# Optimization experiments

Hardware: AMD Instinct MI355X
Metric: run time of the kernel (lower is better)

Reference implementation:

```python
import jax, jax.numpy as jnp
import numpy as np

HID = 2048   # hidden_size
NH = 16      # num_heads
HD = 128     # head_dim
R = 16       # compression_ratio
WIN = 128    # window_size
ROPE = HD // 2  # partial rope dim (resolve_rope_dim with use_partial_rope)
EPS = 1e-6


def rmsnorm(x, w):
    return x * jax.lax.rsqrt(jnp.mean(x * x, axis=-1, keepdims=True) + EPS) * w


def apply_rope(x, pos):
    # x: [..., S, D]; rotate first ROPE dims, pass the rest through.
    half = ROPE // 2
    inv_freq = 1.0 / (10000.0 ** (jnp.arange(half, dtype=jnp.float32) * 2.0 / ROPE))
    ang = pos.astype(jnp.float32)[:, None] * inv_freq[None, :]   # [S, half]
    cos, sin = jnp.cos(ang), jnp.sin(ang)
    x1, x2, rest = x[..., :half], x[..., half:ROPE], x[..., ROPE:]
    return jnp.concatenate([x1 * cos - x2 * sin, x1 * sin + x2 * cos, rest], axis=-1)


def setup_inputs() -> dict:
    key = jax.random.key(0)
    ks = jax.random.split(key, 16)
    s = 0.02
    return {
        "hidden_states": jax.random.normal(ks[0], (1, 2048, HID), jnp.float32),
        "Wq": jax.random.normal(ks[1], (HID, NH * HD), jnp.float32) * s,
        "bq": jnp.zeros((NH * HD,), jnp.float32),
        "Wc": jax.random.normal(ks[2], (HID, 1), jnp.float32) * s,   # learned compressor scores
        "bc": jnp.zeros((1,), jnp.float32),
        "Wk": jax.random.normal(ks[3], (HID, HD), jnp.float32) * s,  # shared compressed KV head
        "bk": jnp.zeros((HD,), jnp.float32),
        "Wv": jax.random.normal(ks[4], (HID, HD), jnp.float32) * s,
        "bv": jnp.zeros((HD,), jnp.float32),
        "Wlk": jax.random.normal(ks[5], (HID, NH * HD), jnp.float32) * s,
        "blk": jnp.zeros((NH * HD,), jnp.float32),
        "Wlv": jax.random.normal(ks[6], (HID, NH * HD), jnp.float32) * s,
        "blv": jnp.zeros((NH * HD,), jnp.float32),
        "qn_w": jnp.ones((HD,), jnp.float32),
        "kn_w": jnp.ones((HD,), jnp.float32),
        "sink_k": jax.random.normal(ks[7], (NH, HD), jnp.float32) * s,
        "sink_v": jax.random.normal(ks[8], (NH, HD), jnp.float32) * s,
        "Wo": jax.random.normal(ks[9], (NH * HD, HID), jnp.float32) * s,
        "bo": jnp.zeros((HID,), jnp.float32),
    }


def reference(hidden_states, Wq, bq, Wc, bc, Wk, bk, Wv, bv, Wlk, blk, Wlv, blv,
              qn_w, kn_w, sink_k, sink_v, Wo, bo):
    B, S, _ = hidden_states.shape
    pos = jnp.arange(S)
    scale = 1.0 / jnp.sqrt(jnp.float32(HD))

    # queries: proj -> heads -> RMSNorm -> partial RoPE
    q = (hidden_states @ Wq + bq).reshape(B, S, NH, HD).transpose(0, 2, 1, 3)  # [B,NH,S,HD]
    q = apply_rope(rmsnorm(q, qn_w), pos)

    # learned weighted KV compression: softmax over each block of R tokens
    C = S // R
    w = jax.nn.softmax((hidden_states @ Wc + bc).reshape(B, C, R), axis=-1)   # [B,C,R]
    entries = jnp.einsum('bcr,bcrh->bch', w, hidden_states.reshape(B, C, R, HID))
    block_ends = jnp.arange(C) * R + (R - 1)

    ck = apply_rope(rmsnorm(entries @ Wk + bk, kn_w), block_ends)  # [B,C,HD] (shared head)
    cv = entries @ Wv + bv                                         # [B,C,HD]

    # dense attention over compressed entries + learnable sink slot
    cs = jnp.einsum('bhsd,bcd->bhsc', q, ck) * scale               # [B,NH,S,C]
    cmask = block_ends[None, :] <= pos[:, None]                    # block fully in past
    cs = jnp.where(cmask, cs, -1e9)
    sink_s = jnp.einsum('bhsd,hd->bhs', q, sink_k) * scale         # sink always attendable
    attn = jax.nn.softmax(jnp.concatenate([cs, sink_s[..., None]], axis=-1), axis=-1)
    ctx_c = (jnp.einsum('bhsc,bcd->bhsd', attn[..., :C], cv)
             + attn[..., C:] * sink_v[None, :, None, :])

    # local sliding-window attention branch
    lk = (hidden_states @ Wlk + blk).reshape(B, S, NH, HD).transpose(0, 2, 1, 3)
    lk = apply_rope(rmsnorm(lk, kn_w), pos)
    lv = (hidden_states @ Wlv + blv).reshape(B, S, NH, HD).transpose(0, 2, 1, 3)
    ls = jnp.einsum('bhsd,bhtd->bhst', q, lk) * scale
    d = pos[:, None] - pos[None, :]
    lmask = (d >= 0) & (d <= WIN)
    lattn = jax.nn.softmax(jnp.where(lmask, ls, -1e9), axis=-1)
    ctx_l = jnp.einsum('bhst,bhtd->bhsd', lattn, lv)

    merged = 0.5 * (ctx_c + ctx_l)                                 # mean over 2 branches
    out = merged.transpose(0, 2, 1, 3).reshape(B, S, NH * HD) @ Wo + bo
    return out
```

## Files before the change

### kernel.cpp

```cpp
#include <hip/hip_runtime.h>


typedef unsigned short u16;
typedef __attribute__((ext_vector_type(8))) short short8;
typedef __attribute__((ext_vector_type(4))) float f32x4;

#define S_LEN 2048
#define HIDN  2048
#define NHEAD 16
#define HDIM  128
#define NCHNK 128
#define NKT   32
#define SCALE 0.08838834764831845f

__device__ __forceinline__ float bf2f(u16 h) {
  return __uint_as_float(((unsigned)h) << 16);
}
__device__ __forceinline__ u16 f2bf(float f) {
  unsigned u = __float_as_uint(f);
  unsigned r = (u + 0x7fffu + ((u >> 16) & 1u)) >> 16;
  return (u16)r;
}

typedef __attribute__((address_space(3))) unsigned int lds_uint;
typedef __attribute__((address_space(1))) unsigned int glb_uint;
__device__ __forceinline__ void gl_lds16(const void* g, void* l) {
  __builtin_amdgcn_global_load_lds((glb_uint*)(unsigned long long)g,
                                   (lds_uint*)(unsigned)(unsigned long long)l,
                                   16, 0, 0);
}

__global__ __launch_bounds__(256) void k_pre(
    const float* __restrict__ Wq, const float* __restrict__ Wlk, const float* __restrict__ Wlv,
    const float* __restrict__ Wo, const float* __restrict__ hs,
    const float* __restrict__ Wc, const float* __restrict__ bc,
    const float* __restrict__ Wk, const float* __restrict__ Wv,
    u16* __restrict__ Wt3, u16* __restrict__ Wt_o, u16* __restrict__ hs_bf,
    float* __restrict__ rope_c, float* __restrict__ rope_s,
    u16* __restrict__ entries_bf, u16* __restrict__ Wkv_t) {
  __shared__ float tile[32][33];
  int z = blockIdx.z;
  int tx = threadIdx.x, ty = threadIdx.y;
  int tid = ty * 32 + tx;
  if (z < 4) {
    const float* src = (z == 0) ? Wq : (z == 1) ? Wlk : (z == 2) ? Wlv : Wo;
    u16* dst = (z < 3) ? (Wt3 + (size_t)z * HIDN * HIDN) : Wt_o;
    int k0 = blockIdx.x * 32, n0 = blockIdx.y * 32;
    #pragma unroll
    for (int i = 0; i < 32; i += 8)
      tile[ty + i][tx] = src[(size_t)(k0 + ty + i) * HIDN + (n0 + tx)];
    __syncthreads();
    #pragma unroll
    for (int i = 0; i < 32; i += 8)
      dst[(size_t)(n0 + ty + i) * HIDN + (k0 + tx)] = f2bf(tile[tx][ty + i]);
    return;
  }
  int bid = blockIdx.y * 64 + blockIdx.x;
  if (z == 4) {
    size_t i4 = ((size_t)bid * 256 + tid) * 4;
    float4 v = *(const float4*)&hs[i4];
    ushort4 o;
    o.x = f2bf(v.x); o.y = f2bf(v.y); o.z = f2bf(v.z); o.w = f2bf(v.w);
    *(ushort4*)&hs_bf[i4] = o;
    return;
  }
  if (bid < 256) {
    int i = bid * 256 + tid;
    int pos = i >> 5, f = i & 31;
    float inv = __expf(-(float)f * (9.210340371976184f / 32.0f));
    float ang = (float)pos * inv;
    rope_c[i] = cosf(ang);
    rope_s[i] = sinf(ang);
    return;
  }
  if (bid < 384) {
    __shared__ float red[16][17];
    __shared__ float wgt[16];
    int c = bid - 256;
    int row = tid >> 4, seg = tid & 15;
    const float* hrow = hs + ((size_t)c * 16 + row) * HIDN;
    float p = 0.f;
    #pragma unroll 8
    for (int k = seg * 128; k < seg * 128 + 128; k += 4) {
      float4 hv = *(const float4*)&hrow[k];
      float4 wv = *(const float4*)&Wc[k];
      p += hv.x * wv.x + hv.y * wv.y + hv.z * wv.z + hv.w * wv.w;
    }
    red[row][seg] = p;
    __syncthreads();
    if (tid < 16) {
      float lg = 0.f;
      #pragma unroll
      for (int j = 0; j < 16; ++j) lg += red[tid][j];
      lg += bc[0];
      float m = lg;
      #pragma unroll
      for (int msk = 1; msk <= 8; msk <<= 1) m = fmaxf(m, __shfl_xor(m, msk));
      float ev = __expf(lg - m);
      float sum = ev;
      #pragma unroll
      for (int msk = 1; msk <= 8; msk <<= 1) sum += __shfl_xor(sum, msk);
      wgt[tid] = ev / sum;
    }
    __syncthreads();
    #pragma unroll
    for (int j = 0; j < 8; ++j) {
      int hb = tid + j * 256;
      float acc = 0.f;
      #pragma unroll
      for (int r = 0; r < 16; ++r)
        acc += wgt[r] * hs[((size_t)c * 16 + r) * HIDN + hb];
      entries_bf[(size_t)c * HIDN + hb] = f2bf(acc);
    }
    return;
  }
  if (bid < 896) {
    int idx = bid - 384;
    int zw = idx >> 8, byw = (idx >> 6) & 3, bxw = idx & 63;
    const float* src = zw ? Wv : Wk;
    u16* dst = Wkv_t + (size_t)zw * HDIM * 2048;
    int k0 = bxw * 32, n0 = byw * 32;
    #pragma unroll
    for (int i = 0; i < 32; i += 8)
      tile[ty + i][tx] = src[(size_t)(k0 + ty + i) * HDIM + (n0 + tx)];
    __syncthreads();
    #pragma unroll
    for (int i = 0; i < 32; i += 8)
      dst[(size_t)(n0 + ty + i) * 2048 + (k0 + tx)] = f2bf(tile[tx][ty + i]);
  }
}

__global__ __launch_bounds__(512, 2) void k_gemm256(
    const u16* __restrict__ A, const u16* __restrict__ Wt3,
    const u16* __restrict__ entries_bf, const u16* __restrict__ Wkv_t,
    const float* __restrict__ bq, const float* __restrict__ blk, const float* __restrict__ blv,
    const float* __restrict__ bk, const float* __restrict__ bv,
    const float* __restrict__ qn_w, const float* __restrict__ kn_w,
    const float* __restrict__ rc, const float* __restrict__ rs,
    u16* __restrict__ q_out, u16* __restrict__ lk_out, u16* __restrict__ lv_t,
    u16* __restrict__ ck_bf, u16* __restrict__ cv_t) {
  __shared__ __align__(16) u16 lds[65536];
  __shared__ float psq[2][4][128];
  int tid = threadIdx.x, lane = tid & 63;
  int wid = tid >> 6;
  int wr = wid >> 2, wc = wid & 3;
  int lin = blockIdx.x;
  int row0, col0, mode;
  const u16 *Ag, *Bg;
  if (lin < 192) {
    int swz = (lin & 7) * 24 + (lin >> 3);
    mode = swz >> 6;
    int tile = swz & 63;
    row0 = (tile & 7) * 256;
    col0 = (tile >> 3) * 256;
    Ag = A; Bg = Wt3 + (size_t)mode * HIDN * HIDN;
  } else {
    mode = 3; row0 = 0; col0 = 0;
    Ag = entries_bf; Bg = Wkv_t;
  }
  int rA = lane & 15, kg = lane >> 4;
  int srow = tid >> 3, sslot = tid & 7;
  int ssl = sslot ^ (srow & 7);

  f32x4 acc[8][4];
  #pragma unroll
  for (int m = 0; m < 8; ++m)
    #pragma unroll
    for (int n = 0; n < 4; ++n) acc[m][n] = (f32x4){0.f, 0.f, 0.f, 0.f};

  auto stage = [&](int b, int i, int kt) {
    int ah;
    const u16* src;
    int rg, dofs;
    if (i < 4) { src = Bg; rg = col0 + i * 64 + srow; dofs = 16384 + i * 4096; }
    else {
      ah = (i == 4) ? 0 : (i == 5) ? 2 : (i == 6) ? 1 : 3;
      src = Ag; rg = row0 + ah * 64 + srow; dofs = ah * 4096;
    }
    gl_lds16(&src[(size_t)rg * HIDN + kt * 64 + ssl * 8],
             &lds[b * 32768 + dofs + tid * 8]);
  };
  auto rdA = [&](int b, int m, int ks) -> short8 {
    int r = wr * 128 + m * 16 + rA;
    int slot = (ks * 4 + kg) ^ (r & 7);
    return *(const short8*)&lds[b * 32768 + r * 64 + slot * 8];
  };
  auto rdB = [&](int b, int n, int ks) -> short8 {
    int r = wc * 64 + n * 16 + rA;
    int slot = (ks * 4 + kg) ^ (r & 7);
    return *(const short8*)&lds[b * 32768 + 16384 + r * 64 + slot * 8];
  };

  #pragma unroll
  for (int i = 0; i < 8; ++i) stage(0, i, 0);

  short8 Af[4], Bf[4][2];
  for (int u = 0; u < NKT; ++u) {
    int cur = u & 1;
    bool pf = (u + 1 < NKT);
    if (pf) {
      #pragma unroll
      for (int i = 0; i < 8; ++i) stage(cur ^ 1, i, u + 1);
    }
    if (pf) asm volatile("s_waitcnt vmcnt(10)" ::: "memory");
    else    asm volatile("s_waitcnt vmcnt(2)" ::: "memory");
    __builtin_amdgcn_sched_barrier(0);
    __builtin_amdgcn_s_barrier();
    #pragma unroll
    for (int n = 0; n < 4; ++n) { Bf[n][0] = rdB(cur, n, 0); Bf[n][1] = rdB(cur, n, 1); }
    #pragma unroll
    for (int m = 0; m < 4; ++m) Af[m] = rdA(cur, m, 0);
    asm volatile("s_waitcnt lgkmcnt(0)" ::: "memory");
    __builtin_amdgcn_sched_barrier(0);
    __builtin_amdgcn_s_setprio(1);
    #pragma unroll
    for (int m = 0; m < 4; ++m)
      #pragma unroll
      for (int n = 0; n < 4; ++n)
        acc[m][n] = __builtin_amdgcn_mfma_f32_16x16x32_bf16(Af[m], Bf[n][0], acc[m][n], 0, 0, 0);
    __builtin_amdgcn_s_setprio(0);
    #pragma unroll
    for (int m = 0; m < 4; ++m) Af[m] = rdA(cur, m, 1);
    asm volatile("s_waitcnt lgkmcnt(0)" ::: "memory");
    __builtin_amdgcn_sched_barrier(0);
    __builtin_amdgcn_s_setprio(1);
    #pragma unroll
    for (int m = 0; m < 4; ++m)
      #pragma unroll
      for (int n = 0; n < 4; ++n)
        acc[m][n] = __builtin_amdgcn_mfma_f32_16x16x32_bf16(Af[m], Bf[n][1], acc[m][n], 0, 0, 0);
    __builtin_amdgcn_s_setprio(0);
    if (pf) asm volatile("s_waitcnt vmcnt(8)" ::: "memory");
    else    asm volatile("s_waitcnt vmcnt(0)" ::: "memory");
    __builtin_amdgcn_sched_barrier(0);
    __builtin_amdgcn_s_barrier();
    #pragma unroll
    for (int m = 0; m < 4; ++m) Af[m] = rdA(cur, m + 4, 0);
    asm volatile("s_waitcnt lgkmcnt(0)" ::: "memory");
    __builtin_amdgcn_sched_barrier(0);
    __builtin_amdgcn_s_setprio(1);
    #pragma unroll
    for (int m = 0; m < 4; ++m)
      #pragma unroll
      for (int n = 0; n < 4; ++n)
        acc[m + 4][n] = __builtin_amdgcn_mfma_f32_16x16x32_bf16(Af[m], Bf[n][0], acc[m + 4][n], 0, 0, 0);
    __builtin_amdgcn_s_setprio(0);
    #pragma unroll
    for (int m = 0; m < 4; ++m) Af[m] = rdA(cur, m + 4, 1);
    asm volatile("s_waitcnt lgkmcnt(0)" ::: "memory");
    __builtin_amdgcn_sched_barrier(0);
    __builtin_amdgcn_s_setprio(1);
    #pragma unroll
    for (int m = 0; m < 4; ++m)
      #pragma unroll
      for (int n = 0; n < 4; ++n)
        acc[m + 4][n] = __builtin_amdgcn_mfma_f32_16x16x32_bf16(Af[m], Bf[n][1], acc[m + 4][n], 0, 0, 0);
    __builtin_amdgcn_s_setprio(0);
    __builtin_amdgcn_s_barrier();
  }

  int cl = rA, rbase = kg * 4;
  #pragma unroll
  for (int n = 0; n < 4; ++n) {
    int dl = wc * 64 + n * 16 + cl;
    float bb;
    if (mode == 3)      bb = (dl < 128) ? bk[dl] : bv[dl - 128];
    else if (mode == 0) bb = bq[col0 + dl];
    else if (mode == 1) bb = blk[col0 + dl];
    else                bb = blv[col0 + dl];
    #pragma unroll
    for (int m = 0; m < 8; ++m)
      #pragma unroll
      for (int j = 0; j < 4; ++j) acc[m][n][j] += bb;
  }

  if (mode == 2) {
    int hh = (col0 >> 7) + (wc >> 1);
    #pragma unroll
    for (int m = 0; m < 8; ++m) {
      int sb = row0 + wr * 128 + m * 16 + rbase;
      #pragma unroll
      for (int n = 0; n < 4; ++n) {
        int dl = (wc & 1) * 64 + n * 16 + cl;
        ushort4 o;
        o.x = f2bf(acc[m][n][0]);
        o.y = f2bf(acc[m][n][1]);
        o.z = f2bf(acc[m][n][2]);
        o.w = f2bf(acc[m][n][3]);
        *(ushort4*)&lv_t[((size_t)hh * HDIM + dl) * S_LEN + sb] = o;
      }
    }
    return;
  }

  bool is_cv = (mode == 3) && (wc >= 2);
  if (!is_cv) {
    #pragma unroll
    for (int m = 0; m < 8; ++m)
      #pragma unroll
      for (int j = 0; j < 4; ++j) {
        float s2 = acc[m][0][j] * acc[m][0][j] + acc[m][1][j] * acc[m][1][j]
                 + acc[m][2][j] * acc[m][2][j] + acc[m][3][j] * acc[m][3][j];
        s2 += __shfl_xor(s2, 1); s2 += __shfl_xor(s2, 2);
        s2 += __shfl_xor(s2, 4); s2 += __shfl_xor(s2, 8);
        if (cl == 0) psq[wr][wc][m * 16 + rbase + j] = s2;
      }
  }
  __syncthreads();
  if (is_cv) {
    if (wr == 0) {
      #pragma unroll
      for (int m = 0; m < 8; ++m) {
        int cchunk = m * 16 + rbase;
        #pragma unroll
        for (int n = 0; n < 4; ++n) {
          int d = (wc - 2) * 64 + n * 16 + cl;
          #pragma unroll
          for (int j = 0; j < 4; ++j)
            cv_t[(size_t)d * NCHNK + cchunk + j] = f2bf(acc[m][n][j]);
        }
      }
    }
    return;
  }
  {
    const float* nw = (mode == 0) ? qn_w : kn_w;
    int hgrp = wc >> 1;
    float nwv[4];
    #pragma unroll
    for (int n = 0; n < 4; ++n) nwv[n] = nw[(wc & 1) * 64 + n * 16 + cl];
    #pragma unroll
    for (int m = 0; m < 8; ++m)
      #pragma unroll
      for (int j = 0; j < 4; ++j) {
        int r16 = m * 16 + rbase + j;
        int s = row0 + wr * 128 + r16;
        bool valid = (mode != 3) || (s < NCHNK);
        int sc2 = valid ? s : 0;
        int pos = (mode == 3) ? (sc2 * 16 + 15) : sc2;
        float rr2 = rsqrtf((psq[wr][hgrp * 2][r16] + psq[wr][hgrp * 2 + 1][r16]) * (1.f / 128.f) + 1e-6f);
        float o[4];
        if ((wc & 1) == 0) {
          #pragma unroll
          for (int n = 0; n < 2; ++n) {
            int i = n * 16 + cl;
            float ca = rc[pos * 32 + i], sa = rs[pos * 32 + i];
            float y1 = acc[m][n][j] * rr2 * nwv[n];
            float y2 = acc[m][n + 2][j] * rr2 * nwv[n + 2];
            o[n] = y1 * ca - y2 * sa;
            o[n + 2] = y1 * sa + y2 * ca;
          }
        } else {
          #pragma unroll
          for (int n = 0; n < 4; ++n) o[n] = acc[m][n][j] * rr2 * nwv[n];
        }
        if (valid) {
          u16* dst;
          if (mode == 3) dst = ck_bf + (size_t)s * HDIM + (wc & 1) * 64;
          else {
            u16* dstb = (mode == 0) ? q_out : lk_out;
            dst = dstb + ((size_t)((col0 >> 7) + hgrp) * S_LEN + s) * HDIM + (wc & 1) * 64;
          }
          #pragma unroll
          for (int n = 0; n < 4; ++n) dst[n * 16 + cl] = f2bf(o[n]);
        }
      }
  }
}

__global__ __launch_bounds__(256, 2) void k_gemm_out(const u16* __restrict__ A, const u16* __restrict__ Bt,
                                                     const float* __restrict__ bias, float* __restrict__ C) {
  __shared__ __align__(16) u16 lds[32768];
  int tid = threadIdx.x, lane = tid & 63;
  int wave = tid >> 6;
  int wr = wave >> 1, wc = wave & 1;
  int lin = blockIdx.x + (blockIdx.y << 4);
  int swz = (lin & 7) * 32 + (lin >> 3);
  int row0 = (swz & 15) * 128, col0 = (swz >> 4) * 128;
  int rA = lane & 15, kg = lane >> 4;
  int srow = tid >> 3, sslot = tid & 7;
  int ssl = sslot ^ (srow & 7);

  f32x4 acc[4][4];
  #pragma unroll
  for (int m = 0; m < 4; ++m)
    #pragma unroll
    for (int n = 0; n < 4; ++n) acc[m][n] = (f32x4){0.f, 0.f, 0.f, 0.f};

  auto stage = [&](int b, int i, int kt) {
    const u16* src = (i < 4) ? Bt : A;
    int rg = ((i < 4) ? col0 : row0) + (i & 3) * 32 + srow;
    int dofs = (i < 4) ? (8192 + i * 2048) : ((i - 4) * 2048);
    gl_lds16(&src[(size_t)rg * HIDN + kt * 64 + ssl * 8],
             &lds[b * 16384 + dofs + tid * 8]);
  };
  auto rdA = [&](int b, int m, int ks) -> short8 {
    int r = wr * 64 + m * 16 + rA;
    int slot = (ks * 4 + kg) ^ (r & 7);
    return *(const short8*)&lds[b * 16384 + r * 64 + slot * 8];
  };
  auto rdB = [&](int b, int n, int ks) -> short8 {
    int r = wc * 64 + n * 16 + rA;
    int slot = (ks * 4 + kg) ^ (r & 7);
    return *(const short8*)&lds[b * 16384 + 8192 + r * 64 + slot * 8];
  };

  #pragma unroll
  for (int i = 0; i < 8; ++i) stage(0, i, 0);

  short8 Af[4], Bf[4][2];
  for (int u = 0; u < NKT; ++u) {
    int cur = u & 1;
    bool pf = (u + 1 < NKT);
    if (pf) {
      #pragma unroll
      for (int i = 0; i < 8; ++i) stage(cur ^ 1, i, u + 1);
    }
    if (pf) asm volatile("s_waitcnt vmcnt(8)" ::: "memory");
    else    asm volatile("s_waitcnt vmcnt(0)" ::: "memory");
    __builtin_amdgcn_sched_barrier(0);
    __builtin_amdgcn_s_barrier();
    #pragma unroll
    for (int n = 0; n < 4; ++n) { Bf[n][0] = rdB(cur, n, 0); Bf[n][1] = rdB(cur, n, 1); }
    #pragma unroll
    for (int m = 0; m < 4; ++m) Af[m] = rdA(cur, m, 0);
    asm volatile("s_waitcnt lgkmcnt(0)" ::: "memory");
    __builtin_amdgcn_sched_barrier(0);
    __builtin_amdgcn_s_setprio(1);
    #pragma unroll
    for (int m = 0; m < 4; ++m)
      #pragma unroll
      for (int n = 0; n < 4; ++n)
        acc[m][n] = __builtin_amdgcn_mfma_f32_16x16x32_bf16(Af[m], Bf[n][0], acc[m][n], 0, 0, 0);
    __builtin_amdgcn_s_setprio(0);
    #pragma unroll
    for (int m = 0; m < 4; ++m) Af[m] = rdA(cur, m, 1);
    asm volatile("s_waitcnt lgkmcnt(0)" ::: "memory");
    __builtin_amdgcn_sched_barrier(0);
    __builtin_amdgcn_s_setprio(1);
    #pragma unroll
    for (int m = 0; m < 4; ++m)
      #pragma unroll
      for (int n = 0; n < 4; ++n)
        acc[m][n] = __builtin_amdgcn_mfma_f32_16x16x32_bf16(Af[m], Bf[n][1], acc[m][n], 0, 0, 0);
    __builtin_amdgcn_s_setprio(0);
    __builtin_amdgcn_s_barrier();
  }

  int rbase = kg * 4, cl = rA;
  #pragma unroll
  for (int m = 0; m < 4; ++m) {
    int rowb = row0 + wr * 64 + m * 16 + rbase;
    #pragma unroll
    for (int n = 0; n < 4; ++n) {
      int col = col0 + wc * 64 + n * 16 + cl;
      float bb = bias[col];
      #pragma unroll
      for (int j = 0; j < 4; ++j)
        C[(size_t)(rowb + j) * HIDN + col] = acc[m][n][j] + bb;
    }
  }
}

__global__ __launch_bounds__(256) void k_attn(const u16* __restrict__ q_bf, const u16* __restrict__ ck_bf,
                                              const u16* __restrict__ cv_t, const float* __restrict__ sink_k,
                                              const float* __restrict__ sink_v,
                                              const u16* __restrict__ lk_bf, const u16* __restrict__ lv_t,
                                              u16* __restrict__ merged) {
  __shared__ __align__(16) u16 kv[21760];
  __shared__ __align__(16) float sc[32][164];
  __shared__ __align__(16) u16 pb[32][168];
  int tid = threadIdx.x, lane = tid & 63, wave = tid >> 6;
  int lin = blockIdx.x;
  int sw = (lin & 7) * 128 + (lin >> 3);
  int s0 = (sw & 63) * 32, h = sw >> 6;
  const size_t hb = (size_t)h * S_LEN * HDIM;
  int rA = lane & 15, kg8 = (lane >> 4) * 8;
  int qt = wave & 1, wg = wave >> 1;

  short8 aq[4];
  #pragma unroll
  for (int c = 0; c < 4; ++c)
    aq[c] = *(const short8*)&q_bf[hb + (size_t)(s0 + qt * 16 + rA) * HDIM + c * 32 + kg8];

  int cmax = s0 / 16 + 2; if (cmax > 128) cmax = 128;
  int nkeys = cmax + 1;
  int nkt = (nkeys + 15) >> 4, nkc = (nkeys + 31) >> 5;

  for (int i = tid; i < cmax * 16; i += 256) {
    int r = i >> 4, cz = (i & 15) * 8;
    *(uint4*)&kv[r * 136 + cz] = *(const uint4*)&ck_bf[r * HDIM + cz];
  }
  if (tid < 128) kv[cmax * 136 + tid] = f2bf(sink_k[h * HDIM + tid]);
  __syncthreads();

  for (int kt = wg; kt < nkt; kt += 2) {
    f32x4 a = (f32x4){0.f, 0.f, 0.f, 0.f};
    #pragma unroll
    for (int c = 0; c < 4; ++c) {
      short8 bk2 = *(const short8*)&kv[(kt * 16 + rA) * 136 + c * 32 + kg8];
      a = __builtin_amdgcn_mfma_f32_16x16x32_bf16(aq[c], bk2, a, 0, 0, 0);
    }
    int rq = qt * 16 + (lane >> 4) * 4;
    #pragma unroll
    for (int j = 0; j < 4; ++j) sc[rq + j][kt * 16 + rA] = a[j];
  }
  __syncthreads();

  {
    int ql = tid >> 3, e = tid & 7, s = s0 + ql;
    int NK = nkc * 32;
    float m = -1e30f;
    for (int i = e; i < NK; i += 8) {
      if (i < nkeys) {
        float raw = sc[ql][i];
        bool valid = (i < cmax) ? (i * 16 + 15 <= s) : true;
        float v = valid ? raw * SCALE : -1e9f;
        sc[ql][i] = v;
        m = fmaxf(m, v);
      }
    }
    m = fmaxf(m, __shfl_xor(m, 1));
    m = fmaxf(m, __shfl_xor(m, 2));
    m = fmaxf(m, __shfl_xor(m, 4));
    float sum = 0.f;
    for (int i = e; i < NK; i += 8) {
      if (i < nkeys) {
        float pv = __expf(sc[ql][i] - m);
        sc[ql][i] = pv;
        sum += pv;
      }
    }
    sum += __shfl_xor(sum, 1);
    sum += __shfl_xor(sum, 2);
    sum += __shfl_xor(sum, 4);
    float inv = 1.f / sum;
    for (int i = e; i < NK; i += 8)
      pb[ql][i] = (i < nkeys) ? f2bf(sc[ql][i] * inv) : (u16)0;
  }
  __syncthreads();

  {
    int d = tid & 127, cstart = tid >> 7;
    u16 sv = f2bf(sink_v[h * HDIM + d]);
    int NC = nkc * 32;
    for (int c = cstart; c < NC; c += 2) {
      u16 v = (c < cmax) ? cv_t[(size_t)d * NCHNK + c] : ((c == cmax) ? sv : (u16)0);
      kv[d * 168 + c] = v;
    }
  }
  __syncthreads();

  f32x4 po_c[4];
  #pragma unroll
  for (int n = 0; n < 4; ++n) po_c[n] = (f32x4){0.f, 0.f, 0.f, 0.f};
  for (int kc = 0; kc < nkc; ++kc) {
    short8 pfrag = *(const short8*)&pb[qt * 16 + rA][kc * 32 + kg8];
    #pragma unroll
    for (int n = 0; n < 4; ++n) {
      short8 av = *(const short8*)&kv[(wg * 64 + n * 16 + rA) * 168 + kc * 32 + kg8];
      po_c[n] = __builtin_amdgcn_mfma_f32_16x16x32_bf16(av, pfrag, po_c[n], 0, 0, 0);
    }
  }
  __syncthreads();

  int tbase = s0 - 128;
  for (int i = tid; i < 160 * 16; i += 256) {
    int r = i >> 4, cz = (i & 15) * 8;
    int t = tbase + r;
    uint4 val = make_uint4(0, 0, 0, 0);
    if (t >= 0) val = *(const uint4*)&lk_bf[hb + (size_t)t * HDIM + cz];
    *(uint4*)&kv[r * 136 + cz] = val;
  }
  __syncthreads();

  for (int kt = wg; kt < 10; kt += 2) {
    f32x4 a = (f32x4){0.f, 0.f, 0.f, 0.f};
    #pragma unroll
    for (int c = 0; c < 4; ++c) {
      short8 bk2 = *(const short8*)&kv[(kt * 16 + rA) * 136 + c * 32 + kg8];
      a = __builtin_amdgcn_mfma_f32_16x16x32_bf16(aq[c], bk2, a, 0, 0, 0);
    }
    int rq = qt * 16 + (lane >> 4) * 4;
    #pragma unroll
    for (int j = 0; j < 4; ++j) sc[rq + j][kt * 16 + rA] = a[j];
  }
  __syncthreads();

  {
    int ql = tid >> 3, e = tid & 7;
    int ilo = 128 - s0; if (ql > ilo) ilo = ql;
    int ihi = ql + 128;
    float m = -1e30f;
    for (int i = e; i < 160; i += 8) {
      bool valid = (i >= ilo) && (i <= ihi);
      float v = valid ? sc[ql][i] * SCALE : -1e9f;
      sc[ql][i] = v;
      m = fmaxf(m, v);
    }
    m = fmaxf(m, __shfl_xor(m, 1));
    m = fmaxf(m, __shfl_xor(m, 2));
    m = fmaxf(m, __shfl_xor(m, 4));
    float sum = 0.f;
    for (int i = e; i < 160; i += 8) {
      float pv = __expf(sc[ql][i] - m);
      sc[ql][i] = pv;
      sum += pv;
    }
    sum += __shfl_xor(sum, 1);
    sum += __shfl_xor(sum, 2);
    sum += __shfl_xor(sum, 4);
    float inv = 1.f / sum;
    for (int i = e; i < 160; i += 8) pb[ql][i] = f2bf(sc[ql][i] * inv);
  }
  __syncthreads();

  {
    int d = tid & 127, c8s = tid >> 7;
    const size_t hbt = (size_t)h * HDIM * S_LEN;
    for (int c8 = c8s; c8 < 20; c8 += 2) {
      int t0 = tbase + c8 * 8;
      uint4 val = make_uint4(0, 0, 0, 0);
      if (t0 >= 0) val = *(const uint4*)&lv_t[hbt + (size_t)d * S_LEN + t0];
      *(uint4*)&kv[d * 168 + c8 * 8] = val;
    }
  }
  __syncthreads();

  {
    f32x4 po[4];
    #pragma unroll
    for (int n = 0; n < 4; ++n) po[n] = (f32x4){0.f, 0.f, 0.f, 0.f};
    #pragma unroll
    for (int kc = 0; kc < 5; ++kc) {
      short8 pfrag = *(const short8*)&pb[qt * 16 + rA][kc * 32 + kg8];
      #pragma unroll
      for (int n = 0; n < 4; ++n) {
        short8 av = *(const short8*)&kv[(wg * 64 + n * 16 + rA) * 168 + kc * 32 + kg8];
        po[n] = __builtin_amdgcn_mfma_f32_16x16x32_bf16(av, pfrag, po[n], 0, 0, 0);
      }
    }
    int q = qt * 16 + rA;
    int s = s0 + q;
    int rb = (lane >> 4) * 4;
    #pragma unroll
    for (int n = 0; n < 4; ++n) {
      int d0 = wg * 64 + n * 16 + rb;
      ushort4 o;
      o.x = f2bf(0.5f * (po[n][0] + po_c[n][0]));
      o.y = f2bf(0.5f * (po[n][1] + po_c[n][1]));
      o.z = f2bf(0.5f * (po[n][2] + po_c[n][2]));
      o.w = f2bf(0.5f * (po[n][3] + po_c[n][3]));
      *(ushort4*)&merged[(size_t)s * HIDN + h * HDIM + d0] = o;
    }
  }
}

extern "C" void kernel_launch(void* const* d_in, const int* in_sizes, int n_in,
                              void* d_out, int out_size, void* d_ws, size_t ws_size,
                              hipStream_t stream) {
  const float* hs     = (const float*)d_in[0];
  const float* Wq     = (const float*)d_in[1];
  const float* bq     = (const float*)d_in[2];
  const float* Wc     = (const float*)d_in[3];
  const float* bc     = (const float*)d_in[4];
  const float* Wk     = (const float*)d_in[5];
  const float* bk     = (const float*)d_in[6];
  const float* Wv     = (const float*)d_in[7];
  const float* bv     = (const float*)d_in[8];
  const float* Wlk    = (const float*)d_in[9];
  const float* blk    = (const float*)d_in[10];
  const float* Wlv    = (const float*)d_in[11];
  const float* blv    = (const float*)d_in[12];
  const float* qn_w   = (const float*)d_in[13];
  const float* kn_w   = (const float*)d_in[14];
  const float* sink_k = (const float*)d_in[15];
  const float* sink_v = (const float*)d_in[16];
  const float* Wo     = (const float*)d_in[17];
  const float* bo     = (const float*)d_in[18];
  float* out = (float*)d_out;

  char* p = (char*)d_ws;
  auto alloc = [&](size_t bytes) {
    char* r = p;
    p += (bytes + 255) & ~(size_t)255;
    return r;
  };
  float* rope_c  = (float*)alloc((size_t)S_LEN * 32 * 4);
  float* rope_s  = (float*)alloc((size_t)S_LEN * 32 * 4);
  u16*   hs_bf   = (u16*)  alloc((size_t)S_LEN * HIDN * 2);
  u16*   Wt3     = (u16*)  alloc((size_t)3 * HIDN * HIDN * 2);
  u16*   Wt_o    = (u16*)  alloc((size_t)HIDN * HIDN * 2);
  u16*   Wkv_t   = (u16*)  alloc((size_t)2 * HDIM * HIDN * 2);
  u16*   ent_bf  = (u16*)  alloc((size_t)256 * HIDN * 2);
  u16*   q_bf    = (u16*)  alloc((size_t)NHEAD * S_LEN * HDIM * 2);
  u16*   lk_bf   = (u16*)  alloc((size_t)NHEAD * S_LEN * HDIM * 2);
  u16*   lv_t    = (u16*)  alloc((size_t)NHEAD * HDIM * S_LEN * 2);
  u16*   ck_bf   = (u16*)  alloc((size_t)NCHNK * HDIM * 2);
  u16*   cv_t    = (u16*)  alloc((size_t)HDIM * NCHNK * 2);
  u16*   merged  = (u16*)  alloc((size_t)S_LEN * HIDN * 2);
  (void)ws_size; (void)in_sizes; (void)n_in; (void)out_size;

  k_pre<<<dim3(64, 64, 6), dim3(32, 8), 0, stream>>>(Wq, Wlk, Wlv, Wo, hs, Wc, bc, Wk, Wv,
                                                     Wt3, Wt_o, hs_bf, rope_c, rope_s,
                                                     ent_bf, Wkv_t);

  k_gemm256<<<193, 512, 0, stream>>>(hs_bf, Wt3, ent_bf, Wkv_t,
                                     bq, blk, blv, bk, bv, qn_w, kn_w,
                                     rope_c, rope_s, q_bf, lk_bf, lv_t, ck_bf, cv_t);

  k_attn<<<1024, 256, 0, stream>>>(q_bf, ck_bf, cv_t, sink_k, sink_v,
                                   lk_bf, lv_t, merged);

  k_gemm_out<<<dim3(16, 16), 256, 0, stream>>>(merged, Wt_o, bo, out);
}
```

Baseline: 216.2 us.

## Simplify GEMM double-buffer schedule and vectorize compressed-V LDS staging

The GEMM main loop now waits for all outstanding global-to-LDS loads and uses a single barrier per k-step, issuing the next tile's prefetch after the barrier. This replaces the earlier split waits and extra barriers, and the staging order changes so A rows load first into contiguous LDS slots. The compressed-V fill in the attention kernel copies full 8-element groups with 16-byte vector loads and stores, handling only the tail per element. The full vmcnt(0) wait may expose more global latency, since the prefetch no longer overlaps the wait.

```diff
diff --git a/kernel.cpp b/kernel.cpp
--- a/kernel.cpp
+++ b/kernel.cpp
@@ -169,16 +169,10 @@
     for (int n = 0; n < 4; ++n) acc[m][n] = (f32x4){0.f, 0.f, 0.f, 0.f};
 
   auto stage = [&](int b, int i, int kt) {
-    int ah;
-    const u16* src;
-    int rg, dofs;
-    if (i < 4) { src = Bg; rg = col0 + i * 64 + srow; dofs = 16384 + i * 4096; }
-    else {
-      ah = (i == 4) ? 0 : (i == 5) ? 2 : (i == 6) ? 1 : 3;
-      src = Ag; rg = row0 + ah * 64 + srow; dofs = ah * 4096;
-    }
+    const u16* src = (i < 4) ? Ag : Bg;
+    int rg = ((i < 4) ? row0 : col0) + ((i & 3) * 64) + srow;
     gl_lds16(&src[(size_t)rg * HIDN + kt * 64 + ssl * 8],
-             &lds[b * 32768 + dofs + tid * 8]);
+             &lds[b * 32768 + i * 4096 + tid * 8]);
   };
   auto rdA = [&](int b, int m, int ks) -> short8 {
     int r = wr * 128 + m * 16 + rA;
@@ -197,15 +191,13 @@
   short8 Af[4], Bf[4][2];
   for (int u = 0; u < NKT; ++u) {
     int cur = u & 1;
-    bool pf = (u + 1 < NKT);
-    if (pf) {
-      #pragma unroll
-      for (int i = 0; i < 8; ++i) stage(cur ^ 1, i, u + 1);
-    }
-    if (pf) asm volatile("s_waitcnt vmcnt(10)" ::: "memory");
-    else    asm volatile("s_waitcnt vmcnt(2)" ::: "memory");
+    asm volatile("s_waitcnt vmcnt(0)" ::: "memory");
     __builtin_amdgcn_sched_barrier(0);
     __builtin_amdgcn_s_barrier();
+    if (u + 1 < NKT) {
+      #pragma unroll
+      for (int i = 0; i < 8; ++i) stage(cur ^ 1, i, u + 1);
+    }
     #pragma unroll
     for (int n = 0; n < 4; ++n) { Bf[n][0] = rdB(cur, n, 0); Bf[n][1] = rdB(cur, n, 1); }
     #pragma unroll
@@ -230,10 +222,6 @@
       for (int n = 0; n < 4; ++n)
         acc[m][n] = __builtin_amdgcn_mfma_f32_16x16x32_bf16(Af[m], Bf[n][1], acc[m][n], 0, 0, 0);
     __builtin_amdgcn_s_setprio(0);
-    if (pf) asm volatile("s_waitcnt vmcnt(8)" ::: "memory");
-    else    asm volatile("s_waitcnt vmcnt(0)" ::: "memory");
-    __builtin_amdgcn_sched_barrier(0);
-    __builtin_amdgcn_s_barrier();
     #pragma unroll
     for (int m = 0; m < 4; ++m) Af[m] = rdA(cur, m + 4, 0);
     asm volatile("s_waitcnt lgkmcnt(0)" ::: "memory");
@@ -256,7 +244,6 @@
       for (int n = 0; n < 4; ++n)
         acc[m + 4][n] = __builtin_amdgcn_mfma_f32_16x16x32_bf16(Af[m], Bf[n][1], acc[m + 4][n], 0, 0, 0);
     __builtin_amdgcn_s_setprio(0);
-    __builtin_amdgcn_s_barrier();
   }
 
   int cl = rA, rbase = kg * 4;
@@ -541,11 +528,15 @@
   __syncthreads();
 
   {
-    int d = tid & 127, cstart = tid >> 7;
+    int d = tid & 127, half = tid >> 7;
+    int ng = cmax >> 3;
+    const u16* srcrow = cv_t + (size_t)d * NCHNK;
+    for (int g = half; g < ng; g += 2)
+      *(uint4*)&kv[d * 168 + g * 8] = *(const uint4*)&srcrow[g * 8];
     u16 sv = f2bf(sink_v[h * HDIM + d]);
     int NC = nkc * 32;
-    for (int c = cstart; c < NC; c += 2) {
-      u16 v = (c < cmax) ? cv_t[(size_t)d * NCHNK + c] : ((c == cmax) ? sv : (u16)0);
+    for (int c = ng * 8 + half; c < NC; c += 2) {
+      u16 v = (c < cmax) ? srcrow[c] : ((c == cmax) ? sv : (u16)0);
       kv[d * 168 + c] = v;
     }
   }
```

Result: faster. 195.7 us (-9.5%).
